# Kernel tuning notes

Measured on AMD Instinct MI355X. Metric: run time of the kernel, lower is better.

The kernel has to match this reference:

```python
import jax, jax.numpy as jnp
import numpy as np

NEG_SLOPE = 0.2
LN_EPS = 1e-5


def setup_inputs() -> dict:
    key = jax.random.key(0)
    k1, k2, k3, k4 = jax.random.split(key, 4)
    N, K, F, O = 100000, 16, 128, 128
    face_features = jax.random.normal(k1, (N, F), dtype=jnp.float32)
    adjacency = jax.random.randint(k2, (N, K), 0, N, dtype=jnp.int64)
    # Linear(2F -> O) params (torch layout: W [O, 2F])
    W = jax.random.normal(k3, (O, 2 * F), dtype=jnp.float32) / np.sqrt(2 * F)
    b = jnp.zeros((O,), dtype=jnp.float32)
    gamma = jnp.ones((O,), dtype=jnp.float32)
    beta = jnp.zeros((O,), dtype=jnp.float32)
    return {"face_features": face_features, "adjacency": adjacency,
            "W": W, "b": b, "gamma": gamma, "beta": beta}


def reference(face_features, adjacency, W, b, gamma, beta):
    # mask for valid neighbors (-1 = padding)
    mask = (adjacency != -1).astype(face_features.dtype)[..., None]  # [N, K, 1]
    neigh = face_features[jnp.clip(adjacency, 0, None)]              # [N, K, F]
    denom = jnp.clip(mask.sum(axis=1), 1.0, None)                    # [N, 1]
    mean_neigh = (neigh * mask).sum(axis=1) / denom                  # [N, F]
    x = jnp.concatenate([face_features, mean_neigh], axis=1)         # [N, 2F]
    h = x @ W.T + b                                                  # [N, O]
    mu = h.mean(axis=-1, keepdims=True)
    var = ((h - mu) ** 2).mean(axis=-1, keepdims=True)
    h = (h - mu) / jnp.sqrt(var + LN_EPS) * gamma + beta
    return jnp.where(h >= 0, h, NEG_SLOPE * h)
```

## Files before the change

### kernel.cpp

```cpp
#include <hip/hip_runtime.h>
#include <stdint.h>

#define F 128
#define KNB 16
#define TWO_F 256
#define ROWS 64
#define THREADS 256
#define HSTR 133
#define LN_EPS 1e-5f
#define NEG_SLOPE 0.2f

typedef unsigned short u16;
typedef __bf16 bf16x8 __attribute__((ext_vector_type(8)));
typedef float f32x4 __attribute__((ext_vector_type(4)));

union BF8 { bf16x8 v; u16 us[8]; uint4 u4; };

__device__ __forceinline__ float b2f(u16 u) {
    union { float f; uint32_t i; } v; v.i = ((uint32_t)u) << 16; return v.f;
}
__device__ __forceinline__ u16 f2b(float f) {
    union { float f; uint32_t i; } v; v.f = f;
    uint32_t r = (v.i + 0x7FFFu + ((v.i >> 16) & 1u)) >> 16;
    return (u16)r;
}

extern "C" __global__ void cast_f32_bf16(const float* __restrict__ src,
                                         u16* __restrict__ dst, int n8) {
    const int i = blockIdx.x * blockDim.x + threadIdx.x;
    if (i >= n8) return;
    const float4* s = (const float4*)src + (size_t)i * 2;
    const float4 a = s[0], b = s[1];
    BF8 o;
    o.us[0] = f2b(a.x); o.us[1] = f2b(a.y); o.us[2] = f2b(a.z); o.us[3] = f2b(a.w);
    o.us[4] = f2b(b.x); o.us[5] = f2b(b.y); o.us[6] = f2b(b.z); o.us[7] = f2b(b.w);
    ((uint4*)dst)[i] = o.u4;
}

template <int FEAT_BF, int W_BF>
__global__ __launch_bounds__(THREADS, 4)
void gnn_fused(const float* __restrict__ feat_f32, const u16* __restrict__ feat_bf,
               const int* __restrict__ adj,
               const float* __restrict__ W_f32, const u16* __restrict__ W_bf,
               const float* __restrict__ bias, const float* __restrict__ gamma,
               const float* __restrict__ beta,
               float* __restrict__ out, int N)
{
    __shared__ float hb[ROWS * HSTR];

    const int tid  = threadIdx.x;
    const int wave = tid >> 6;
    const int lane = tid & 63;
    const int ln15 = lane & 15;
    const int quad = lane >> 4;
    const int fb   = quad * 8;
    const int rb   = wave * 16;

    const long rowA  = (long)blockIdx.x * ROWS + rb + ln15;
    const bool rok   = rowA < (long)N;
    const long rsafe = rok ? rowA : 0;

    int idx[16];
    {
        const int4* ap = (const int4*)(adj + rsafe * KNB);
        const int4 a0 = ap[0], a1 = ap[1], a2 = ap[2], a3 = ap[3];
        idx[0]  = a0.x; idx[1]  = a0.y; idx[2]  = a0.z; idx[3]  = a0.w;
        idx[4]  = a1.x; idx[5]  = a1.y; idx[6]  = a1.z; idx[7]  = a1.w;
        idx[8]  = a2.x; idx[9]  = a2.y; idx[10] = a2.z; idx[11] = a2.w;
        idx[12] = a3.x; idx[13] = a3.y; idx[14] = a3.z; idx[15] = a3.w;
    }

    bf16x8 afrag[8];
    if (FEAT_BF) {
        const u16* orow = feat_bf + rsafe * F + fb;
        #pragma unroll
        for (int j = 0; j < 4; ++j)
            afrag[j] = *(const bf16x8*)(orow + j * 32);
    } else {
        const float* orow = feat_f32 + rsafe * F + fb;
        #pragma unroll
        for (int j = 0; j < 4; ++j) {
            const float4 p0 = *(const float4*)(orow + j * 32);
            const float4 p1 = *(const float4*)(orow + j * 32 + 4);
            BF8 o;
            o.us[0] = f2b(p0.x); o.us[1] = f2b(p0.y); o.us[2] = f2b(p0.z); o.us[3] = f2b(p0.w);
            o.us[4] = f2b(p1.x); o.us[5] = f2b(p1.y); o.us[6] = f2b(p1.z); o.us[7] = f2b(p1.w);
            afrag[j] = o.v;
        }
    }

    float acc[32];
    #pragma unroll
    for (int t = 0; t < 32; ++t) acc[t] = 0.f;
    int cnt = 0;

    if (rok) {
        for (int k = 0; k < KNB; ++k) {
            const int id = idx[k];
            if (id >= 0 && id < N) {
                ++cnt;
                if (FEAT_BF) {
                    const u16* nb = feat_bf + (size_t)id * F + fb;
                    #pragma unroll
                    for (int j = 0; j < 4; ++j) {
                        BF8 u; u.u4 = *(const uint4*)(nb + j * 32);
                        #pragma unroll
                        for (int t = 0; t < 8; ++t) acc[j * 8 + t] += b2f(u.us[t]);
                    }
                } else {
                    const float* nb = feat_f32 + (size_t)id * F + fb;
                    #pragma unroll
                    for (int j = 0; j < 4; ++j) {
                        const float4 p0 = *(const float4*)(nb + j * 32);
                        const float4 p1 = *(const float4*)(nb + j * 32 + 4);
                        acc[j * 8 + 0] += p0.x; acc[j * 8 + 1] += p0.y;
                        acc[j * 8 + 2] += p0.z; acc[j * 8 + 3] += p0.w;
                        acc[j * 8 + 4] += p1.x; acc[j * 8 + 5] += p1.y;
                        acc[j * 8 + 6] += p1.z; acc[j * 8 + 7] += p1.w;
                    }
                }
            }
        }
    }
    const float scale = 1.f / (float)(cnt > 0 ? cnt : 1);

    #pragma unroll
    for (int j = 0; j < 4; ++j) {
        BF8 o;
        #pragma unroll
        for (int t = 0; t < 8; ++t) o.us[t] = f2b(acc[j * 8 + t] * scale);
        afrag[4 + j] = o.v;
    }

    f32x4 accf[8];
    #pragma unroll
    for (int c = 0; c < 8; ++c) accf[c] = (f32x4){0.f, 0.f, 0.f, 0.f};

    #pragma unroll
    for (int ks = 0; ks < 8; ++ks) {
        #pragma unroll
        for (int c = 0; c < 8; ++c) {
            bf16x8 bfrag;
            if (W_BF) {
                bfrag = *(const bf16x8*)(W_bf + (size_t)(c * 16 + ln15) * TWO_F + fb + ks * 32);
            } else {
                const float* wr = W_f32 + (size_t)(c * 16 + ln15) * TWO_F + fb + ks * 32;
                const float4 a = *(const float4*)wr, b = *(const float4*)(wr + 4);
                BF8 o;
                o.us[0] = f2b(a.x); o.us[1] = f2b(a.y); o.us[2] = f2b(a.z); o.us[3] = f2b(a.w);
                o.us[4] = f2b(b.x); o.us[5] = f2b(b.y); o.us[6] = f2b(b.z); o.us[7] = f2b(b.w);
                bfrag = o.v;
            }
            accf[c] = __builtin_amdgcn_mfma_f32_16x16x32_bf16(afrag[ks], bfrag, accf[c], 0, 0, 0);
        }
    }

    float bval[8];
    #pragma unroll
    for (int c = 0; c < 8; ++c) bval[c] = bias[c * 16 + ln15];

    #pragma unroll
    for (int c = 0; c < 8; ++c) {
        #pragma unroll
        for (int t = 0; t < 4; ++t) {
            const int rr = quad * 4 + t;
            hb[(rb + rr) * HSTR + c * 16 + ln15] = accf[c][t] + bval[c];
        }
    }
    asm volatile("s_waitcnt lgkmcnt(0)" ::: "memory");
    __builtin_amdgcn_sched_barrier(0);

    const int er = lane >> 2;
    const int eq = lane & 3;
    const float* hr = hb + (rb + er) * HSTR + eq * 32;
    float sum = 0.f, sq = 0.f;
    #pragma unroll
    for (int t = 0; t < 32; ++t) { const float v = hr[t]; sum += v; sq += v * v; }
    sum += __shfl_xor(sum, 1); sq += __shfl_xor(sq, 1);
    sum += __shfl_xor(sum, 2); sq += __shfl_xor(sq, 2);

    const float mu   = sum * (1.f / 128.f);
    const float var  = sq * (1.f / 128.f) - mu * mu;
    const float rsig = rsqrtf(fmaxf(var, 0.f) + LN_EPS);

    const long org = (long)blockIdx.x * ROWS + rb + er;
    if (org < N) {
        const int cb = eq * 32;
        float* orow = out + org * F + cb;
        #pragma unroll
        for (int j = 0; j < 8; ++j) {
            const float4 g  = *(const float4*)(gamma + cb + j * 4);
            const float4 bt = *(const float4*)(beta  + cb + j * 4);
            float4 o;
            o.x = (hr[j * 4 + 0] - mu) * rsig * g.x + bt.x;
            o.y = (hr[j * 4 + 1] - mu) * rsig * g.y + bt.y;
            o.z = (hr[j * 4 + 2] - mu) * rsig * g.z + bt.z;
            o.w = (hr[j * 4 + 3] - mu) * rsig * g.w + bt.w;
            o.x = (o.x >= 0.f) ? o.x : NEG_SLOPE * o.x;
            o.y = (o.y >= 0.f) ? o.y : NEG_SLOPE * o.y;
            o.z = (o.z >= 0.f) ? o.z : NEG_SLOPE * o.z;
            o.w = (o.w >= 0.f) ? o.w : NEG_SLOPE * o.w;
            *(float4*)(orow + j * 4) = o;
        }
    }
}

extern "C" void kernel_launch(void* const* d_in, const int* in_sizes, int n_in,
                              void* d_out, int out_size, void* d_ws, size_t ws_size,
                              hipStream_t stream) {
    const float* feat  = (const float*)d_in[0];
    const int*   adj   = (const int*)d_in[1];
    const float* W     = (const float*)d_in[2];
    const float* bias  = (const float*)d_in[3];
    const float* gamma = (const float*)d_in[4];
    const float* beta  = (const float*)d_in[5];
    float* out = (float*)d_out;

    const int N = in_sizes[0] / F;
    const size_t needW = (size_t)TWO_F * F * sizeof(u16);
    const size_t needF = (size_t)N * F * sizeof(u16);
    u16* wsW = (u16*)d_ws;
    u16* wsF = (u16*)((char*)d_ws + needW);

    const int mode = (ws_size >= needW + needF) ? 2 : (ws_size >= needW ? 1 : 0);

    if (mode >= 1) {
        const int n8 = TWO_F * F / 8;
        cast_f32_bf16<<<dim3((n8 + 255) / 256), dim3(256), 0, stream>>>(W, wsW, n8);
    }
    if (mode == 2) {
        const int n8 = N * F / 8;
        cast_f32_bf16<<<dim3((n8 + 255) / 256), dim3(256), 0, stream>>>(feat, wsF, n8);
    }

    const int blocks = (N + ROWS - 1) / ROWS;
    if (mode == 2) {
        gnn_fused<1, 1><<<dim3(blocks), dim3(THREADS), 0, stream>>>(feat, wsF, adj, W, wsW, bias, gamma, beta, out, N);
    } else if (mode == 1) {
        gnn_fused<0, 1><<<dim3(blocks), dim3(THREADS), 0, stream>>>(feat, wsF, adj, W, wsW, bias, gamma, beta, out, N);
    } else {
        gnn_fused<0, 0><<<dim3(blocks), dim3(THREADS), 0, stream>>>(feat, wsF, adj, W, wsW, bias, gamma, beta, out, N);
    }
}
```

Before: 237.8 us.

## Split neighbor gather-mean into a separate kernel before the GEMM+LayerNorm kernel

Adds a dedicated gather_mean kernel in which four threads per row accumulate 16 bf16 neighbor rows and write a bf16 mean buffer. A new gnn_split kernel then reads that buffer, runs the MFMA GEMM, LayerNorm and LeakyReLU. The aim is to decouple the latency-bound random gather from the MFMA stage so each kernel can reach higher occupancy. The cost is an extra N×F bf16 workspace round trip, one more launch, and a second bf16 rounding of the mean.

```diff
diff --git a/kernel.cpp b/kernel.cpp
--- a/kernel.cpp
+++ b/kernel.cpp
@@ -35,6 +35,149 @@
     o.us[0] = f2b(a.x); o.us[1] = f2b(a.y); o.us[2] = f2b(a.z); o.us[3] = f2b(a.w);
     o.us[4] = f2b(b.x); o.us[5] = f2b(b.y); o.us[6] = f2b(b.z); o.us[7] = f2b(b.w);
     ((uint4*)dst)[i] = o.u4;
+}
+
+extern "C" __global__ __launch_bounds__(256, 5)
+void gather_mean(const u16* __restrict__ feat_bf, const int* __restrict__ adj,
+                 u16* __restrict__ mean_bf, int N)
+{
+    const int gt  = blockIdx.x * 256 + threadIdx.x;
+    const int row = gt >> 2;
+    if (row >= N) return;
+    const int fb = (gt & 3) * 32;
+
+    int idx[16];
+    {
+        const int4* ap = (const int4*)(adj + (size_t)row * KNB);
+        const int4 a0 = ap[0], a1 = ap[1], a2 = ap[2], a3 = ap[3];
+        idx[0]  = a0.x; idx[1]  = a0.y; idx[2]  = a0.z; idx[3]  = a0.w;
+        idx[4]  = a1.x; idx[5]  = a1.y; idx[6]  = a1.z; idx[7]  = a1.w;
+        idx[8]  = a2.x; idx[9]  = a2.y; idx[10] = a2.z; idx[11] = a2.w;
+        idx[12] = a3.x; idx[13] = a3.y; idx[14] = a3.z; idx[15] = a3.w;
+    }
+
+    float acc[32];
+    #pragma unroll
+    for (int t = 0; t < 32; ++t) acc[t] = 0.f;
+    int cnt = 0;
+
+    for (int k = 0; k < KNB; ++k) {
+        const int id = idx[k];
+        if (id >= 0 && id < N) {
+            ++cnt;
+            const u16* nb = feat_bf + (size_t)id * F + fb;
+            #pragma unroll
+            for (int j = 0; j < 4; ++j) {
+                BF8 u; u.u4 = *(const uint4*)(nb + j * 8);
+                #pragma unroll
+                for (int t = 0; t < 8; ++t) acc[j * 8 + t] += b2f(u.us[t]);
+            }
+        }
+    }
+
+    const float scale = 1.f / (float)(cnt > 0 ? cnt : 1);
+    uint4* dst = (uint4*)(mean_bf + (size_t)row * F + fb);
+    #pragma unroll
+    for (int j = 0; j < 4; ++j) {
+        BF8 o;
+        #pragma unroll
+        for (int t = 0; t < 8; ++t) o.us[t] = f2b(acc[j * 8 + t] * scale);
+        dst[j] = o.u4;
+    }
+}
+
+extern "C" __global__ __launch_bounds__(THREADS, 4)
+void gnn_split(const u16* __restrict__ feat_bf, const u16* __restrict__ mean_bf,
+               const u16* __restrict__ W_bf,
+               const float* __restrict__ bias, const float* __restrict__ gamma,
+               const float* __restrict__ beta,
+               float* __restrict__ out, int N)
+{
+    __shared__ float hb[ROWS * HSTR];
+
+    const int tid  = threadIdx.x;
+    const int wave = tid >> 6;
+    const int lane = tid & 63;
+    const int ln15 = lane & 15;
+    const int quad = lane >> 4;
+    const int fb   = quad * 8;
+    const int rb   = wave * 16;
+
+    const long rowA  = (long)blockIdx.x * ROWS + rb + ln15;
+    const bool rok   = rowA < (long)N;
+    const long rsafe = rok ? rowA : 0;
+
+    bf16x8 afrag[8];
+    {
+        const u16* orow = feat_bf + rsafe * F + fb;
+        const u16* mrow = mean_bf + rsafe * F + fb;
+        #pragma unroll
+        for (int j = 0; j < 4; ++j) afrag[j]     = *(const bf16x8*)(orow + j * 32);
+        #pragma unroll
+        for (int j = 0; j < 4; ++j) afrag[4 + j] = *(const bf16x8*)(mrow + j * 32);
+    }
+
+    f32x4 accf[8];
+    #pragma unroll
+    for (int c = 0; c < 8; ++c) accf[c] = (f32x4){0.f, 0.f, 0.f, 0.f};
+
+    #pragma unroll
+    for (int ks = 0; ks < 8; ++ks) {
+        #pragma unroll
+        for (int c = 0; c < 8; ++c) {
+            const bf16x8 bfrag = *(const bf16x8*)(W_bf + (size_t)(c * 16 + ln15) * TWO_F + fb + ks * 32);
+            accf[c] = __builtin_amdgcn_mfma_f32_16x16x32_bf16(afrag[ks], bfrag, accf[c], 0, 0, 0);
+        }
+    }
+
+    float bval[8];
+    #pragma unroll
+    for (int c = 0; c < 8; ++c) bval[c] = bias[c * 16 + ln15];
+
+    #pragma unroll
+    for (int c = 0; c < 8; ++c) {
+        #pragma unroll
+        for (int t = 0; t < 4; ++t) {
+            const int rr = quad * 4 + t;
+            hb[(rb + rr) * HSTR + c * 16 + ln15] = accf[c][t] + bval[c];
+        }
+    }
+    asm volatile("s_waitcnt lgkmcnt(0)" ::: "memory");
+    __builtin_amdgcn_sched_barrier(0);
+
+    const int er = lane >> 2;
+    const int eq = lane & 3;
+    const float* hr = hb + (rb + er) * HSTR + eq * 32;
+    float sum = 0.f, sq = 0.f;
+    #pragma unroll
+    for (int t = 0; t < 32; ++t) { const float v = hr[t]; sum += v; sq += v * v; }
+    sum += __shfl_xor(sum, 1); sq += __shfl_xor(sq, 1);
+    sum += __shfl_xor(sum, 2); sq += __shfl_xor(sq, 2);
+
+    const float mu   = sum * (1.f / 128.f);
+    const float var  = sq * (1.f / 128.f) - mu * mu;
+    const float rsig = rsqrtf(fmaxf(var, 0.f) + LN_EPS);
+
+    const long org = (long)blockIdx.x * ROWS + rb + er;
+    if (org < N) {
+        const int cb = eq * 32;
+        float* orow = out + org * F + cb;
+        #pragma unroll
+        for (int j = 0; j < 8; ++j) {
+            const float4 g  = *(const float4*)(gamma + cb + j * 4);
+            const float4 bt = *(const float4*)(beta  + cb + j * 4);
+            float4 o;
+            o.x = (hr[j * 4 + 0] - mu) * rsig * g.x + bt.x;
+            o.y = (hr[j * 4 + 1] - mu) * rsig * g.y + bt.y;
+            o.z = (hr[j * 4 + 2] - mu) * rsig * g.z + bt.z;
+            o.w = (hr[j * 4 + 3] - mu) * rsig * g.w + bt.w;
+            o.x = (o.x >= 0.f) ? o.x : NEG_SLOPE * o.x;
+            o.y = (o.y >= 0.f) ? o.y : NEG_SLOPE * o.y;
+            o.z = (o.z >= 0.f) ? o.z : NEG_SLOPE * o.z;
+            o.w = (o.w >= 0.f) ? o.w : NEG_SLOPE * o.w;
+            *(float4*)(orow + j * 4) = o;
+        }
+    }
 }
 
 template <int FEAT_BF, int W_BF>
@@ -219,11 +362,25 @@
     const int N = in_sizes[0] / F;
     const size_t needW = (size_t)TWO_F * F * sizeof(u16);
     const size_t needF = (size_t)N * F * sizeof(u16);
+    const size_t needM = (size_t)N * F * sizeof(u16);
     u16* wsW = (u16*)d_ws;
     u16* wsF = (u16*)((char*)d_ws + needW);
+    u16* wsM = (u16*)((char*)d_ws + needW + needF);
+
+    const int blocks = (N + ROWS - 1) / ROWS;
+
+    if (ws_size >= needW + needF + needM) {
+        const int n8w = TWO_F * F / 8;
+        cast_f32_bf16<<<dim3((n8w + 255) / 256), dim3(256), 0, stream>>>(W, wsW, n8w);
+        const int n8f = N * F / 8;
+        cast_f32_bf16<<<dim3((n8f + 255) / 256), dim3(256), 0, stream>>>(feat, wsF, n8f);
+        const int gth = N * 4;
+        gather_mean<<<dim3((gth + 255) / 256), dim3(256), 0, stream>>>(wsF, adj, wsM, N);
+        gnn_split<<<dim3(blocks), dim3(THREADS), 0, stream>>>(wsF, wsM, wsW, bias, gamma, beta, out, N);
+        return;
+    }
 
     const int mode = (ws_size >= needW + needF) ? 2 : (ws_size >= needW ? 1 : 0);
-
     if (mode >= 1) {
         const int n8 = TWO_F * F / 8;
         cast_f32_bf16<<<dim3((n8 + 255) / 256), dim3(256), 0, stream>>>(W, wsW, n8);
@@ -232,8 +389,6 @@
         const int n8 = N * F / 8;
         cast_f32_bf16<<<dim3((n8 + 255) / 256), dim3(256), 0, stream>>>(feat, wsF, n8);
     }
-
-    const int blocks = (N + ROWS - 1) / ROWS;
     if (mode == 2) {
         gnn_fused<1, 1><<<dim3(blocks), dim3(THREADS), 0, stream>>>(feat, wsF, adj, W, wsW, bias, gamma, beta, out, N);
     } else if (mode == 1) {
```

Result: slower. 243.5 us (+2.4%).
